# Kernel optimization log

Measured on AMD Instinct MI355X. Metric: run time of the kernel, lower is better.

The kernel has to match this reference:

```python
import jax, jax.numpy as jnp
import numpy as np

DIM = 128
N_HEADS = 4
HEAD_DIM = DIM // N_HEADS  # 32
RANK = 8
SCALING = 16.0 / RANK      # alpha / rank = 2.0
ROPE_BASE = 10000.0
INV_SQRT_HD = 1.0 / float(np.sqrt(HEAD_DIM))


def _rope(x, cos, sin):
    # x: [B, S, H, D]; interleaved-pair rotation matching torch view(..., -1, 2)
    B, S, H, D = x.shape
    xr = x.reshape(B, S, H, D // 2, 2)
    x1, x2 = xr[..., 0], xr[..., 1]
    c = cos[None, :, None, :]  # [1, S, 1, D/2]
    s = sin[None, :, None, :]
    out = jnp.stack([x1 * c - x2 * s, x1 * s + x2 * c], axis=-1)
    return out.reshape(B, S, H, D)


def setup_inputs() -> dict:
    key = jax.random.key(0)
    ks = jax.random.split(key, 11)
    B, S = 128, 256
    w = lambda k, shp: jax.random.normal(k, shp, dtype=jnp.float32) * 0.05
    return {
        "x": jax.random.normal(ks[0], (B, S, DIM), dtype=jnp.float32),
        "wq": w(ks[1], (DIM, DIM)),
        "wk": w(ks[2], (DIM, DIM)),
        "wv": w(ks[3], (DIM, DIM)),
        "wo": w(ks[4], (DIM, DIM)),
        "lora_A_q": w(ks[5], (RANK, DIM)),
        "lora_B_q": w(ks[6], (DIM, RANK)),
        "lora_A_k": w(ks[7], (RANK, DIM)),
        "lora_B_k": w(ks[8], (DIM, RANK)),
        "lora_A_v": w(ks[9], (RANK, DIM)),
        "lora_B_v": w(ks[10], (DIM, RANK)),
    }


def reference(x, wq, wk, wv, wo, lora_A_q, lora_B_q, lora_A_k, lora_B_k,
              lora_A_v, lora_B_v):
    B, S, _ = x.shape
    # RoPE tables (HEAD_DIM split into pairs)
    pos = jnp.arange(S, dtype=jnp.float32)
    inv_freq = 1.0 / (ROPE_BASE ** (jnp.arange(0, HEAD_DIM, 2, dtype=jnp.float32) / HEAD_DIM))
    freqs = pos[:, None] * inv_freq[None, :]  # [S, HEAD_DIM/2]
    cos, sin = jnp.cos(freqs), jnp.sin(freqs)

    def proj(w, A, Bm):
        # base linear (no bias) + LoRA low-rank delta (dropout = eval identity)
        return x @ w.T + (x @ A.T @ Bm.T) * SCALING

    q = proj(wq, lora_A_q, lora_B_q).reshape(B, S, N_HEADS, HEAD_DIM)
    k = proj(wk, lora_A_k, lora_B_k).reshape(B, S, N_HEADS, HEAD_DIM)
    v = proj(wv, lora_A_v, lora_B_v).reshape(B, S, N_HEADS, HEAD_DIM)

    q = _rope(q, cos, sin).transpose(0, 2, 1, 3)  # [B, H, S, D]
    k = _rope(k, cos, sin).transpose(0, 2, 1, 3)
    v = v.transpose(0, 2, 1, 3)

    scores = jnp.einsum('bhqd,bhkd->bhqk', q, k) * INV_SQRT_HD
    causal = jnp.triu(jnp.ones((S, S), dtype=bool), k=1)
    scores = jnp.where(causal[None, None], -jnp.inf, scores)
    attn = jax.nn.softmax(scores, axis=-1)

    out = jnp.einsum('bhqk,bhkd->bhqd', attn, v)
    out = out.transpose(0, 2, 1, 3).reshape(B, S, DIM)
    return out @ wo.T
```

## Files before the change

### kernel.cpp

```cpp
#include <hip/hip_runtime.h>
#include <math.h>

typedef __attribute__((ext_vector_type(8))) short short8;
typedef __attribute__((ext_vector_type(4))) float floatx4;

#define NH 4
#define HD 32
#define DIM 128
#define SEQ 256
#define BATCH 128
#define BS (BATCH*SEQ)
#define RANK 8
#define SCALING 2.0f
#define INV_SQRT_HD 0.17677669529663687f
#define LOG2E 1.4426950408889634f

#if __has_builtin(__builtin_amdgcn_exp2f)
#define EXP2F __builtin_amdgcn_exp2f
#else
#define EXP2F exp2f
#endif

#define QB_OFF  (0ull)
#define KB_OFF  (8ull<<20)
#define VT_OFF  (16ull<<20)
#define XB_OFF  (24ull<<20)
#define WE_OFF  (32ull<<20)
#define TAB_OFF (33ull<<20)

static __device__ __forceinline__ unsigned short f2bf(float f) {
    unsigned u = __float_as_uint(f);
    return (unsigned short)((u + 0x7FFFu + ((u >> 16) & 1u)) >> 16);
}
static __device__ __forceinline__ unsigned packbf(float lo, float hi) {
    unsigned ua = __float_as_uint(lo), ub = __float_as_uint(hi);
    ua += 0x7FFFu + ((ua >> 16) & 1u);
    ub += 0x7FFFu + ((ub >> 16) & 1u);
    return __builtin_amdgcn_perm(ub, ua, 0x07060302);
}

__global__ __launch_bounds__(256) void prep_kernel(
    const float* __restrict__ x,
    const float* __restrict__ wq, const float* __restrict__ wk,
    const float* __restrict__ wv, const float* __restrict__ wo,
    const float* __restrict__ Aq, const float* __restrict__ Bq,
    const float* __restrict__ Ak, const float* __restrict__ Bk,
    const float* __restrict__ Av, const float* __restrict__ Bv,
    unsigned short* __restrict__ weffL, float* __restrict__ tab,
    unsigned short* __restrict__ xbL)
{
    const int bid = blockIdx.x, tid = threadIdx.x;
    if (bid < 128) {
        int t = bid * 256 + tid;
        int m    = t >> 13;
        int kc   = (t >> 11) & 3;
        int s    = (t >> 8) & 7;
        int lane = (t >> 2) & 63;
        int e    = t & 3;
        int m16 = lane & 15, quad = lane >> 4;
        int row = (m < 3) ? ((s >> 1) * 32 + 2 * m16 + (s & 1)) : (s * 16 + m16);
        int col = kc * 32 + quad * 8 + 2 * e;
        const float* W = m == 0 ? wq : (m == 1 ? wk : (m == 2 ? wv : wo));
        const float* A  = m == 0 ? Aq : (m == 1 ? Ak : Av);
        const float* Bm = m == 0 ? Bq : (m == 1 ? Bk : Bv);
        float v0 = W[row * DIM + col], v1 = W[row * DIM + col + 1];
        if (m < 3) {
            float s0 = 0.f, s1 = 0.f;
#pragma unroll
            for (int r = 0; r < RANK; r++) {
                float br = Bm[row * RANK + r];
                s0 += br * A[r * DIM + col];
                s1 += br * A[r * DIM + col + 1];
            }
            v0 += SCALING * s0;
            v1 += SCALING * s1;
        }
        if (m == 0) { v0 *= INV_SQRT_HD * LOG2E; v1 *= INV_SQRT_HD * LOG2E; }
        ((unsigned*)weffL)[t] = packbf(v0, v1);
    } else if (bid < 144) {
        int gid = (bid - 128) * 256 + tid;
        int spos = gid >> 4, i = gid & 15;
        float invf = exp2f(-0.83048202f * (float)i);
        float ang = (float)spos * invf;
        float c, s;
        sincosf(ang, &s, &c);
        tab[gid * 2]     = c;
        tab[gid * 2 + 1] = s;
    } else {
        int t = (bid - 144) * 256 + tid;
        int g    = t >> 8;
        int kc   = (t >> 6) & 3;
        int lane = t & 63;
        int m16 = lane & 15, quad = lane >> 4;
        const float* xp = x + (size_t)(g * 16 + m16) * DIM + kc * 32 + quad * 8;
        float4 f0 = *(const float4*)xp;
        float4 f1 = *(const float4*)(xp + 4);
        uint4 o;
        o.x = packbf(f0.x, f0.y); o.y = packbf(f0.z, f0.w);
        o.z = packbf(f1.x, f1.y); o.w = packbf(f1.z, f1.w);
        *(uint4*)(xbL + (size_t)t * 8) = o;
    }
}

#define VSTU 68
__global__ __launch_bounds__(256) void qkv_kernel(
    const unsigned short* __restrict__ xbL, const unsigned short* __restrict__ weffL,
    const float* __restrict__ tab,
    unsigned* __restrict__ qb, unsigned* __restrict__ kb,
    unsigned short* __restrict__ vtL)
{
    __shared__ unsigned vs_u[64 * VSTU];

    const int which = blockIdx.y;
    const unsigned short* W = weffL + which * DIM * DIM;

    const int tid = threadIdx.x;
    const int w = __builtin_amdgcn_readfirstlane(tid >> 6);
    const int lane = tid & 63;
    const int m16 = lane & 15, quad = lane >> 4;
    const int g = blockIdx.x * 4 + w;
    const int b = g >> 4;

    short8 afrag[4];
#pragma unroll
    for (int kc = 0; kc < 4; kc++)
        afrag[kc] = *(const short8*)(xbL + ((size_t)(g * 4 + kc) * 64 + lane) * 8);

    floatx4 acc_e[NH], acc_o[NH];
#pragma unroll
    for (int h = 0; h < NH; h++) {
        acc_e[h] = (floatx4){0.f, 0.f, 0.f, 0.f};
        acc_o[h] = (floatx4){0.f, 0.f, 0.f, 0.f};
    }

#pragma unroll
    for (int kc = 0; kc < 4; kc++) {
#pragma unroll
        for (int h = 0; h < NH; h++) {
            const unsigned short* base = W + ((kc * 8 + h * 2) * 64 + lane) * 8;
            short8 be = *(const short8*)base;
            short8 bo = *(const short8*)(base + 512);
            acc_e[h] = __builtin_amdgcn_mfma_f32_16x16x32_bf16(afrag[kc], be, acc_e[h], 0, 0, 0);
            acc_o[h] = __builtin_amdgcn_mfma_f32_16x16x32_bf16(afrag[kc], bo, acc_o[h], 0, 0, 0);
        }
    }

    if (which < 2) {
        unsigned* outp = which == 0 ? qb : kb;
        const int sposq = (g & 15) * 16 + quad * 4;
#pragma unroll
        for (int r = 0; r < 4; r++) {
            int spos = sposq + r;
            float2 cs = *(const float2*)(tab + ((size_t)spos * 16 + m16) * 2);
#pragma unroll
            for (int h = 0; h < NH; h++) {
                float e = acc_e[h][r], o = acc_o[h][r];
                outp[((size_t)(b * NH + h) * SEQ + spos) * (HD / 2) + m16] =
                    packbf(e * cs.x - o * cs.y, e * cs.y + o * cs.x);
            }
        }
    } else {
        const int cloc = w >> 1;
        const int sig0 = (w & 1);
#pragma unroll
        for (int r = 0; r < 4; r++) {
            int sig = 8 * quad + 2 * r + sig0;
            int col = cloc * 32 + (sig ^ ((m16 & 3) << 3));
#pragma unroll
            for (int h = 0; h < NH; h++)
                vs_u[(h * 16 + m16) * VSTU + col] = packbf(acc_e[h][r], acc_o[h][r]);
        }
        __syncthreads();
        const int cb = ((blockIdx.x * 64) & 255) >> 5;
        const size_t bhbase = (size_t)(b * NH) * 8;
#pragma unroll
        for (int it = 0; it < 4; it++) {
            int f = it * 256 + tid;
            int c_l = f >> 9;
            int h   = (f >> 7) & 3;
            int p   = (f >> 6) & 1;
            int ln  = f & 63;
            int fm16 = ln & 15, fq = ln >> 4;
            const unsigned* src = vs_u + (h * 16 + fm16) * VSTU + c_l * 32
                                + ((fq ^ (fm16 & 3)) * 8);
            uint4 a = *(const uint4*)src;
            uint4 bb = *(const uint4*)(src + 4);
            unsigned sel = p ? 0x07060302u : 0x05040100u;
            uint4 o;
            o.x = __builtin_amdgcn_perm(a.y,  a.x,  sel);
            o.y = __builtin_amdgcn_perm(a.w,  a.z,  sel);
            o.z = __builtin_amdgcn_perm(bb.y, bb.x, sel);
            o.w = __builtin_amdgcn_perm(bb.w, bb.z, sel);
            *(uint4*)(vtL + (((bhbase + h * 8 + cb + c_l) * 2 + p) * 512 + ln * 8)) = o;
        }
    }
}

#define PBU 20
#define OS_STRIDE 136
__global__ __launch_bounds__(256) void attn_kernel(
    const unsigned short* __restrict__ qbs, const unsigned short* __restrict__ kbs,
    const unsigned short* __restrict__ vtL, const unsigned short* __restrict__ woL,
    float* __restrict__ out)
{
    __shared__ unsigned pbuf_u[4 * 2 * 16 * PBU];
    __shared__ unsigned short os[32 * OS_STRIDE];

    const int p  = blockIdx.x;
    const int b  = blockIdx.y;
    const int tid = threadIdx.x;
    const int w = __builtin_amdgcn_readfirstlane(tid >> 6);
    const int lane = tid & 63;
    const int m16 = lane & 15, quad = lane >> 4;

    const size_t bh = (size_t)(b * NH + w);
    const unsigned short* krow = kbs + bh * SEQ * HD;
    const unsigned short* vbase = vtL + bh * 8 * 1024;

    const short ob = (short)0x3F80;
    const short8 bones = {ob, ob, ob, ob, ob, ob, ob, ob};
    const floatx4 z4 = (floatx4){0.f, 0.f, 0.f, 0.f};
    unsigned* pw = pbuf_u + (w * 2) * 16 * PBU;

    for (int half = 0; half < 2; half++) {
        const int qt = half ? p : (7 - p);
        const int q0 = qt * 32;
        const unsigned short* qrow = qbs + (bh * SEQ + q0) * HD;

        short8 aq[2];
#pragma unroll
        for (int qs = 0; qs < 2; qs++)
            aq[qs] = *(const short8*)(qrow + (size_t)(qs * 16 + m16) * HD + quad * 8);

        floatx4 o_e[2], o_o[2], o_l[2];
#pragma unroll
        for (int qs = 0; qs < 2; qs++) { o_e[qs] = z4; o_o[qs] = z4; o_l[qs] = z4; }

        const int nchunks = qt + 1;
        short8 cbk0, cbk1, cbve, cbvo, nbk0, nbk1, nbve, nbvo;
        {
            cbk0 = *(const short8*)(krow + (size_t)m16 * HD + quad * 8);
            cbk1 = *(const short8*)(krow + (size_t)(16 + m16) * HD + quad * 8);
            const unsigned short* vp = vbase + lane * 8;
            cbve = *(const short8*)vp;
            cbvo = *(const short8*)(vp + 512);
        }

        for (int c = 0; c < nchunks; c++) {
            const int cn = (c + 1 < nchunks) ? c + 1 : c;
            {
                const unsigned short* kp = krow + (size_t)cn * 32 * HD;
                nbk0 = *(const short8*)(kp + (size_t)m16 * HD + quad * 8);
                nbk1 = *(const short8*)(kp + (size_t)(16 + m16) * HD + quad * 8);
                const unsigned short* vp = vbase + (size_t)cn * 1024 + lane * 8;
                nbve = *(const short8*)vp;
                nbvo = *(const short8*)(vp + 512);
            }
            const int k0 = c * 32;
            const int kg0 = k0 + m16, kg1 = k0 + 16 + m16;
#pragma unroll
            for (int qs = 0; qs < 2; qs++) {
                floatx4 s0 = __builtin_amdgcn_mfma_f32_16x16x32_bf16(aq[qs], cbk0, z4, 0, 0, 0);
                floatx4 s1 = __builtin_amdgcn_mfma_f32_16x16x32_bf16(aq[qs], cbk1, z4, 0, 0, 0);
                unsigned* pq = pw + qs * 16 * PBU;
                const int qg = q0 + qs * 16 + quad * 4;
#pragma unroll
                for (int r = 0; r < 4; r++) {
                    float p0 = (kg0 <= qg + r) ? EXP2F(s0[r]) : 0.f;
                    float p1 = (kg1 <= qg + r) ? EXP2F(s1[r]) : 0.f;
                    pq[(quad * 4 + r) * PBU + m16] = packbf(p0, p1);
                }
                const unsigned short* pqs = (const unsigned short*)pq;
                short8 ap = *(const short8*)(pqs + m16 * (PBU * 2) + quad * 8);
                o_e[qs] = __builtin_amdgcn_mfma_f32_16x16x32_bf16(ap, cbve, o_e[qs], 0, 0, 0);
                o_o[qs] = __builtin_amdgcn_mfma_f32_16x16x32_bf16(ap, cbvo, o_o[qs], 0, 0, 0);
                o_l[qs] = __builtin_amdgcn_mfma_f32_16x16x32_bf16(ap, bones, o_l[qs], 0, 0, 0);
            }
            cbk0 = nbk0; cbk1 = nbk1; cbve = nbve; cbvo = nbvo;
        }

        if (half) __syncthreads();
        unsigned* osu = (unsigned*)os;
#pragma unroll
        for (int qs = 0; qs < 2; qs++)
#pragma unroll
            for (int r = 0; r < 4; r++) {
                float inv = 1.f / o_l[qs][r];
                osu[(qs * 16 + quad * 4 + r) * (OS_STRIDE / 2) + w * 16 + m16] =
                    packbf(o_e[qs][r] * inv, o_o[qs][r] * inv);
            }
        __syncthreads();

        const int tw = (w & 1) * 16;
        const int dbase = (w >> 1) * 64;

        short8 af[4];
#pragma unroll
        for (int kc = 0; kc < 4; kc++)
            af[kc] = *(const short8*)(os + (tw + m16) * OS_STRIDE + kc * 32 + quad * 8);

        floatx4 acc[4];
#pragma unroll
        for (int nt = 0; nt < 4; nt++) acc[nt] = z4;
#pragma unroll
        for (int kc = 0; kc < 4; kc++)
#pragma unroll
            for (int nt = 0; nt < 4; nt++) {
                short8 bf = *(const short8*)(woL + ((kc * 8 + (w >> 1) * 4 + nt) * 64 + lane) * 8);
                acc[nt] = __builtin_amdgcn_mfma_f32_16x16x32_bf16(af[kc], bf, acc[nt], 0, 0, 0);
            }

#pragma unroll
        for (int nt = 0; nt < 4; nt++)
#pragma unroll
            for (int r = 0; r < 4; r++)
                out[(size_t)(b * SEQ + q0 + tw + quad * 4 + r) * DIM
                    + dbase + nt * 16 + m16] = acc[nt][r];
    }
}

extern "C" void kernel_launch(void* const* d_in, const int* in_sizes, int n_in,
                              void* d_out, int out_size, void* d_ws, size_t ws_size,
                              hipStream_t stream)
{
    const float* x  = (const float*)d_in[0];
    const float* wq = (const float*)d_in[1];
    const float* wk = (const float*)d_in[2];
    const float* wv = (const float*)d_in[3];
    const float* wo = (const float*)d_in[4];
    const float* Aq = (const float*)d_in[5];
    const float* Bq = (const float*)d_in[6];
    const float* Ak = (const float*)d_in[7];
    const float* Bk = (const float*)d_in[8];
    const float* Av = (const float*)d_in[9];
    const float* Bv = (const float*)d_in[10];
    float* out = (float*)d_out;
    char* ws = (char*)d_ws;

    unsigned*       qb    = (unsigned*)(ws + QB_OFF);
    unsigned*       kb    = (unsigned*)(ws + KB_OFF);
    unsigned short* vtL   = (unsigned short*)(ws + VT_OFF);
    unsigned short* xbL   = (unsigned short*)(ws + XB_OFF);
    unsigned short* weffL = (unsigned short*)(ws + WE_OFF);
    float*          tab   = (float*)(ws + TAB_OFF);

    prep_kernel<<<144 + 2048, 256, 0, stream>>>(
        x, wq, wk, wv, wo, Aq, Bq, Ak, Bk, Av, Bv, weffL, tab, xbL);
    qkv_kernel<<<dim3(BS / 64, 3), 256, 0, stream>>>(xbL, weffL, tab, qb, kb, vtL);
    attn_kernel<<<dim3(4, BATCH), 256, 0, stream>>>(
        (const unsigned short*)qb, (const unsigned short*)kb, vtL,
        weffL + 3 * DIM * DIM, out);
}
```

Measured before the change: 118.2 us.

## Fuse Q projection and RoPE into attention kernel, drop Q buffer

The Q projection and its RoPE rotation move from the QKV kernel into the attention kernel. Each wave computes its head's Q tile with MFMA from the bf16 x layout, rotates it, and stages it through the per-wave LDS buffer to rebuild the A fragment. This removes the global write and read of the Q buffer and one third of the QKV grid. The cost is extra MFMA work, x and weight loads inside the attention kernel, and a reuse of pbuf with no explicit wave-level barrier, relying on in-order LDS access within a wave.

```diff
diff --git a/kernel.cpp b/kernel.cpp
--- a/kernel.cpp
+++ b/kernel.cpp
@@ -21,7 +21,6 @@
 #define EXP2F exp2f
 #endif
 
-#define QB_OFF  (0ull)
 #define KB_OFF  (8ull<<20)
 #define VT_OFF  (16ull<<20)
 #define XB_OFF  (24ull<<20)
@@ -106,12 +105,11 @@
 __global__ __launch_bounds__(256) void qkv_kernel(
     const unsigned short* __restrict__ xbL, const unsigned short* __restrict__ weffL,
     const float* __restrict__ tab,
-    unsigned* __restrict__ qb, unsigned* __restrict__ kb,
-    unsigned short* __restrict__ vtL)
+    unsigned* __restrict__ kb, unsigned short* __restrict__ vtL)
 {
     __shared__ unsigned vs_u[64 * VSTU];
 
-    const int which = blockIdx.y;
+    const int which = blockIdx.y + 1;
     const unsigned short* W = weffL + which * DIM * DIM;
 
     const int tid = threadIdx.x;
@@ -145,8 +143,7 @@
         }
     }
 
-    if (which < 2) {
-        unsigned* outp = which == 0 ? qb : kb;
+    if (which == 1) {
         const int sposq = (g & 15) * 16 + quad * 4;
 #pragma unroll
         for (int r = 0; r < 4; r++) {
@@ -155,7 +152,7 @@
 #pragma unroll
             for (int h = 0; h < NH; h++) {
                 float e = acc_e[h][r], o = acc_o[h][r];
-                outp[((size_t)(b * NH + h) * SEQ + spos) * (HD / 2) + m16] =
+                kb[((size_t)(b * NH + h) * SEQ + spos) * (HD / 2) + m16] =
                     packbf(e * cs.x - o * cs.y, e * cs.y + o * cs.x);
             }
         }
@@ -199,8 +196,9 @@
 #define PBU 20
 #define OS_STRIDE 136
 __global__ __launch_bounds__(256) void attn_kernel(
-    const unsigned short* __restrict__ qbs, const unsigned short* __restrict__ kbs,
-    const unsigned short* __restrict__ vtL, const unsigned short* __restrict__ woL,
+    const unsigned short* __restrict__ xbL, const unsigned short* __restrict__ weffL,
+    const float* __restrict__ tab,
+    const unsigned short* __restrict__ kbs, const unsigned short* __restrict__ vtL,
     float* __restrict__ out)
 {
     __shared__ unsigned pbuf_u[4 * 2 * 16 * PBU];
@@ -216,6 +214,8 @@
     const size_t bh = (size_t)(b * NH + w);
     const unsigned short* krow = kbs + bh * SEQ * HD;
     const unsigned short* vbase = vtL + bh * 8 * 1024;
+    const unsigned short* Wq = weffL;
+    const unsigned short* woL = weffL + (size_t)3 * DIM * DIM;
 
     const short ob = (short)0x3F80;
     const short8 bones = {ob, ob, ob, ob, ob, ob, ob, ob};
@@ -225,12 +225,29 @@
     for (int half = 0; half < 2; half++) {
         const int qt = half ? p : (7 - p);
         const int q0 = qt * 32;
-        const unsigned short* qrow = qbs + (bh * SEQ + q0) * HD;
 
         short8 aq[2];
 #pragma unroll
-        for (int qs = 0; qs < 2; qs++)
-            aq[qs] = *(const short8*)(qrow + (size_t)(qs * 16 + m16) * HD + quad * 8);
+        for (int qs = 0; qs < 2; qs++) {
+            const int g = b * 16 + qt * 2 + qs;
+            floatx4 ae = z4, ao = z4;
+#pragma unroll
+            for (int kc = 0; kc < 4; kc++) {
+                short8 xf = *(const short8*)(xbL + ((size_t)(g * 4 + kc) * 64 + lane) * 8);
+                const unsigned short* bp = Wq + ((size_t)(kc * 8 + w * 2) * 64 + lane) * 8;
+                ae = __builtin_amdgcn_mfma_f32_16x16x32_bf16(xf, *(const short8*)bp, ae, 0, 0, 0);
+                ao = __builtin_amdgcn_mfma_f32_16x16x32_bf16(xf, *(const short8*)(bp + 512), ao, 0, 0, 0);
+            }
+            const int sbase = q0 + qs * 16 + quad * 4;
+#pragma unroll
+            for (int r = 0; r < 4; r++) {
+                float2 cs = *(const float2*)(tab + ((size_t)(sbase + r) * 16 + m16) * 2);
+                float e = ae[r], o = ao[r];
+                pw[(quad * 4 + r) * PBU + m16] =
+                    packbf(e * cs.x - o * cs.y, e * cs.y + o * cs.x);
+            }
+            aq[qs] = *(const short8*)((const unsigned short*)pw + m16 * (PBU * 2) + quad * 8);
+        }
 
         floatx4 o_e[2], o_o[2], o_l[2];
 #pragma unroll
@@ -337,7 +354,6 @@
     float* out = (float*)d_out;
     char* ws = (char*)d_ws;
 
-    unsigned*       qb    = (unsigned*)(ws + QB_OFF);
     unsigned*       kb    = (unsigned*)(ws + KB_OFF);
     unsigned short* vtL   = (unsigned short*)(ws + VT_OFF);
     unsigned short* xbL   = (unsigned short*)(ws + XB_OFF);
@@ -346,8 +362,7 @@
 
     prep_kernel<<<144 + 2048, 256, 0, stream>>>(
         x, wq, wk, wv, wo, Aq, Bq, Ak, Bk, Av, Bv, weffL, tab, xbL);
-    qkv_kernel<<<dim3(BS / 64, 3), 256, 0, stream>>>(xbL, weffL, tab, qb, kb, vtL);
+    qkv_kernel<<<dim3(BS / 64, 2), 256, 0, stream>>>(xbL, weffL, tab, kb, vtL);
     attn_kernel<<<dim3(4, BATCH), 256, 0, stream>>>(
-        (const unsigned short*)qb, (const unsigned short*)kb, vtL,
-        weffL + 3 * DIM * DIM, out);
-}
+        xbL, weffL, tab, (const unsigned short*)kb, vtL, out);
+}
```

New measurement: 119.7 us. Within noise of the previous version (+1.2%).
